# Optimization experiments

Hardware: AMD Instinct MI355X
Metric: run time of the kernel (lower is better)

Reference implementation:

```python
import jax, jax.numpy as jnp
import numpy as np

N_HEADS = 16
D_EMBED = 1024
D_HEADS = D_EMBED // N_HEADS


def setup_inputs() -> dict:
    key = jax.random.key(0)
    k1, k2, k3, k4, k5 = jax.random.split(key, 5)
    B, S = 4, 2048
    x = jax.random.normal(k1, (B, S, D_EMBED), dtype=jnp.float32)
    s_in = 1.0 / np.sqrt(D_EMBED)
    in_proj_w = jax.random.normal(k2, (3 * D_EMBED, D_EMBED), dtype=jnp.float32) * s_in
    in_proj_b = jax.random.normal(k3, (3 * D_EMBED,), dtype=jnp.float32) * 0.01
    out_proj_w = jax.random.normal(k4, (D_EMBED, D_EMBED), dtype=jnp.float32) * s_in
    out_proj_b = jax.random.normal(k5, (D_EMBED,), dtype=jnp.float32) * 0.01
    return {"x": x, "in_proj_w": in_proj_w, "in_proj_b": in_proj_b,
            "out_proj_w": out_proj_w, "out_proj_b": out_proj_b}


def reference(x, in_proj_w, in_proj_b, out_proj_w, out_proj_b):
    B, S, D = x.shape
    # in_proj: Linear(d, 3d); torch chunks output as (k, q, v) in that order
    qkv = jnp.einsum('bsd,ed->bse', x, in_proj_w) + in_proj_b  # [B,S,3D]
    k, q, v = jnp.split(qkv, 3, axis=-1)
    # reshape to heads: [B, H, S, Dh]
    def to_heads(t):
        return t.reshape(B, S, N_HEADS, D_HEADS).transpose(0, 2, 1, 3)
    q, k, v = to_heads(q), to_heads(k), to_heads(v)
    scale = 1.0 / np.sqrt(D_HEADS)
    w = jnp.einsum('bhqd,bhkd->bhqk', q, k) * scale  # [B,H,S,S]
    w = jax.nn.softmax(w, axis=-1)
    score = jnp.einsum('bhqk,bhkd->bhqd', w, v)  # [B,H,S,Dh]
    score = score.transpose(0, 2, 1, 3).reshape(B, S, D)
    out = jnp.einsum('bsd,ed->bse', score, out_proj_w) + out_proj_b
    return out
```

## Files before the change

kernel.cpp:

```cpp
#include <hip/hip_runtime.h>

typedef __attribute__((ext_vector_type(8))) __bf16 bf16x8;
typedef __attribute__((ext_vector_type(4))) float  f32x4;
typedef __attribute__((ext_vector_type(4))) unsigned short us4;

#define QK_SCALE 0.180336880111112f

__device__ __forceinline__ unsigned short f2bf(float f) {
    unsigned u = __float_as_uint(f);
    u += 0x7fffu + ((u >> 16) & 1u);
    return (unsigned short)(u >> 16);
}

__device__ __forceinline__ void gload_lds16(const void* g, void* l) {
    __builtin_amdgcn_global_load_lds((const __attribute__((address_space(1))) void*)g,
                                     (__attribute__((address_space(3))) void*)l, 16, 0, 0);
}

template <int CTRL>
__device__ __forceinline__ float dpp_mov(float x) {
    return __int_as_float(__builtin_amdgcn_update_dpp(0, __float_as_int(x), CTRL, 0xf, 0xf, true));
}
__device__ __forceinline__ float rmax16(float v) {
    v = fmaxf(v, dpp_mov<0x121>(v));
    v = fmaxf(v, dpp_mov<0x122>(v));
    v = fmaxf(v, dpp_mov<0x124>(v));
    v = fmaxf(v, dpp_mov<0x128>(v));
    return v;
}
__device__ __forceinline__ float rsum16(float v) {
    v += dpp_mov<0x121>(v);
    v += dpp_mov<0x122>(v);
    v += dpp_mov<0x124>(v);
    v += dpp_mov<0x128>(v);
    return v;
}

__global__ __launch_bounds__(256) void f32_to_bf16_k(const float* __restrict__ in,
                                                     unsigned short* __restrict__ out, int n) {
    int i = (blockIdx.x * 256 + threadIdx.x) * 4;
    if (i + 3 < n) {
        float4 v = *(const float4*)(in + i);
        us4 o;
        o.x = f2bf(v.x); o.y = f2bf(v.y); o.z = f2bf(v.z); o.w = f2bf(v.w);
        *(us4*)(out + i) = o;
    }
}

__global__ __launch_bounds__(256) void cvt_w1_k(const float* __restrict__ in,
                                                unsigned short* __restrict__ out) {
    int i = (blockIdx.x * 256 + threadIdx.x) * 4;
    float4 v = *(const float4*)(in + i);
    const int row = i >> 10;
    const float s = (row >= 1024 && row < 2048) ? QK_SCALE : 1.0f;
    us4 o;
    o.x = f2bf(v.x * s); o.y = f2bf(v.y * s); o.z = f2bf(v.z * s); o.w = f2bf(v.w * s);
    *(us4*)(out + i) = o;
}

template <int OUTF, int QS>
__global__ __launch_bounds__(256, 2) void gemm_bt(const unsigned short* __restrict__ A,
                                                  const unsigned short* __restrict__ B,
                                                  const float* __restrict__ bias,
                                                  void* __restrict__ Cv,
                                                  int M, int N, int K) {
    __shared__ unsigned short As[4 * 128 * 8];
    __shared__ unsigned short Bs[4 * 128 * 8];
    const int t = threadIdx.x;
    const int lane = t & 63;
    const int w = t >> 6;
    const int wr = w >> 1, wc = w & 1;
    const int lhi = lane >> 4, llo = lane & 15;
    const int bm = blockIdx.y, bn = blockIdx.x;

    f32x4 acc[4][4] = {};

    const unsigned short* Ag = A + (size_t)(bm * 128) * K;
    const unsigned short* Bg = B + (size_t)(bn * 128) * K;

    const int r0 = t & 127, kc0 = t >> 7;
    const int r1 = (256 + t) & 127, kc1 = (256 + t) >> 7;
    const int wbase = (t & ~63) * 8;

    const int KT = K >> 5;
    for (int kt = 0; kt < KT; ++kt) {
        const int k0 = kt * 32;
        gload_lds16(Ag + (size_t)r0 * K + k0 + kc0 * 8, As + wbase);
        gload_lds16(Ag + (size_t)r1 * K + k0 + kc1 * 8, As + 2048 + wbase);
        gload_lds16(Bg + (size_t)r0 * K + k0 + kc0 * 8, Bs + wbase);
        gload_lds16(Bg + (size_t)r1 * K + k0 + kc1 * 8, Bs + 2048 + wbase);
        __syncthreads();

        bf16x8 af[4], bfr[4];
#pragma unroll
        for (int mi = 0; mi < 4; ++mi)
            af[mi] = *(const bf16x8*)(As + lhi * 1024 + (wr * 64 + mi * 16 + llo) * 8);
#pragma unroll
        for (int ni = 0; ni < 4; ++ni)
            bfr[ni] = *(const bf16x8*)(Bs + lhi * 1024 + (wc * 64 + ni * 16 + llo) * 8);
#pragma unroll
        for (int mi = 0; mi < 4; ++mi)
#pragma unroll
            for (int ni = 0; ni < 4; ++ni)
                acc[mi][ni] = __builtin_amdgcn_mfma_f32_16x16x32_bf16(af[mi], bfr[ni], acc[mi][ni], 0, 0, 0);
        __syncthreads();
    }

    const int rowb = bm * 128 + wr * 64;
    const int colb = bn * 128 + wc * 64;
#pragma unroll
    for (int mi = 0; mi < 4; ++mi) {
#pragma unroll
        for (int ni = 0; ni < 4; ++ni) {
            const int col = colb + ni * 16 + llo;
            float bv = bias[col];
            if (QS) bv = (col >= 1024 && col < 2048) ? bv * QK_SCALE : bv;
#pragma unroll
            for (int r = 0; r < 4; ++r) {
                const int row = rowb + mi * 16 + lhi * 4 + r;
                const float v = acc[mi][ni][r] + bv;
                if (OUTF == 0) ((unsigned short*)Cv)[(size_t)row * N + col] = f2bf(v);
                else           ((float*)Cv)[(size_t)row * N + col] = v;
            }
        }
    }
}

__global__ __launch_bounds__(256) void attn_k(const unsigned short* __restrict__ qkv,
                                              unsigned short* __restrict__ score) {
    __shared__ unsigned short Ks[2][4096];
    __shared__ unsigned short Vt[64 * 88];
    __shared__ unsigned short Pl[4][16 * 88];

    const int t = threadIdx.x;
    const int lane = t & 63;
    const int w = t >> 6;
    const int lhi = lane >> 4, llo = lane & 15;
    const int b = blockIdx.y >> 4, h = blockIdx.y & 15;
    const int q0 = blockIdx.x * 128;

    const unsigned short* kvb = qkv + (size_t)b * 2048 * 3072 + h * 64;

    bf16x8 qf[2][2];
#pragma unroll
    for (int mf = 0; mf < 2; ++mf) {
        const unsigned short* qp = qkv + (size_t)(b * 2048 + q0 + w * 32 + mf * 16 + llo) * 3072
                                   + 1024 + h * 64 + lhi * 8;
        qf[mf][0] = *(const bf16x8*)qp;
        qf[mf][1] = *(const bf16x8*)(qp + 32);
    }

    f32x4 oacc[2][4] = {};
    float m_[2][4], l_[2][4];
#pragma unroll
    for (int mf = 0; mf < 2; ++mf)
#pragma unroll
        for (int r = 0; r < 4; ++r) { m_[mf][r] = -1e30f; l_[mf][r] = 0.f; }

    const int vp = t & 31, vdc = t >> 5;
    bf16x8 vr0, vr1;

    auto issueK = [&](int kt, int buf) {
        const unsigned short* g = kvb + (size_t)(kt * 64 + (t & 63)) * 3072 + (t >> 6) * 8;
        gload_lds16(g,      &Ks[buf][(t & ~63) * 8]);
        gload_lds16(g + 32, &Ks[buf][2048 + (t & ~63) * 8]);
    };
    auto issueV = [&](int kt) {
        const unsigned short* g = kvb + 2048 + (size_t)(kt * 64 + 2 * vp) * 3072 + vdc * 8;
        vr0 = *(const bf16x8*)g;
        vr1 = *(const bf16x8*)(g + 3072);
    };
    auto writeVt = [&]() {
        union { bf16x8 v; unsigned short u[8]; } a, c;
        a.v = vr0; c.v = vr1;
        unsigned int* V32 = (unsigned int*)Vt;
#pragma unroll
        for (int j = 0; j < 8; ++j)
            V32[(vdc * 8 + j) * 44 + vp] = (unsigned int)a.u[j] | ((unsigned int)c.u[j] << 16);
    };

    issueK(0, 0);
    __builtin_amdgcn_sched_barrier(0);
    issueV(0);

    for (int kt = 0; kt < 32; ++kt) {
        const int cur = kt & 1;
        if (kt < 31) issueK(kt + 1, cur ^ 1);
        __builtin_amdgcn_sched_barrier(0);
        writeVt();
        if (kt < 31) issueV(kt + 1);
        asm volatile("s_waitcnt lgkmcnt(0)" ::: "memory");
        __builtin_amdgcn_sched_barrier(0);
        __builtin_amdgcn_s_barrier();
        __builtin_amdgcn_sched_barrier(0);

        f32x4 sa[2][4] = {};
#pragma unroll
        for (int ds = 0; ds < 2; ++ds) {
#pragma unroll
            for (int nf = 0; nf < 4; ++nf) {
                bf16x8 kb = *(const bf16x8*)(&Ks[cur][(ds * 4 + lhi) * 512 + (nf * 16 + llo) * 8]);
                sa[0][nf] = __builtin_amdgcn_mfma_f32_16x16x32_bf16(qf[0][ds], kb, sa[0][nf], 0, 0, 0);
                sa[1][nf] = __builtin_amdgcn_mfma_f32_16x16x32_bf16(qf[1][ds], kb, sa[1][nf], 0, 0, 0);
            }
        }

        bf16x8 pa[2][2];
        unsigned short* pw = Pl[w];
#pragma unroll
        for (int mf = 0; mf < 2; ++mf) {
#pragma unroll
            for (int r = 0; r < 4; ++r) {
                float pm = fmaxf(fmaxf(sa[mf][0][r], sa[mf][1][r]), fmaxf(sa[mf][2][r], sa[mf][3][r]));
                pm = rmax16(pm);
                const float mn = fmaxf(m_[mf][r], pm);
                const float c = __builtin_amdgcn_exp2f(m_[mf][r] - mn);
                m_[mf][r] = mn;
                const float p0 = __builtin_amdgcn_exp2f(sa[mf][0][r] - mn);
                const float p1 = __builtin_amdgcn_exp2f(sa[mf][1][r] - mn);
                const float p2 = __builtin_amdgcn_exp2f(sa[mf][2][r] - mn);
                const float p3 = __builtin_amdgcn_exp2f(sa[mf][3][r] - mn);
                sa[mf][0][r] = p0; sa[mf][1][r] = p1; sa[mf][2][r] = p2; sa[mf][3][r] = p3;
                l_[mf][r] = l_[mf][r] * c + (p0 + p1 + p2 + p3);
#pragma unroll
                for (int nf = 0; nf < 4; ++nf) oacc[mf][nf][r] *= c;
            }
#pragma unroll
            for (int nf = 0; nf < 4; ++nf) {
                const int pc = (nf * 16 + llo + (lhi << 4)) & 63;
#pragma unroll
                for (int r = 0; r < 4; ++r)
                    pw[(lhi * 4 + r) * 88 + pc] = f2bf(sa[mf][nf][r]);
            }
            const int xr = (llo & 12) << 2;
            pa[mf][0] = *(const bf16x8*)(pw + llo * 88 + ((lhi * 8 + xr) & 63));
            pa[mf][1] = *(const bf16x8*)(pw + llo * 88 + ((32 + lhi * 8 + xr) & 63));
        }

#pragma unroll
        for (int ks = 0; ks < 2; ++ks) {
#pragma unroll
            for (int nf = 0; nf < 4; ++nf) {
                bf16x8 vb = *(const bf16x8*)(Vt + (nf * 16 + llo) * 88 + ks * 32 + lhi * 8);
                oacc[0][nf] = __builtin_amdgcn_mfma_f32_16x16x32_bf16(pa[0][ks], vb, oacc[0][nf], 0, 0, 0);
                oacc[1][nf] = __builtin_amdgcn_mfma_f32_16x16x32_bf16(pa[1][ks], vb, oacc[1][nf], 0, 0, 0);
            }
        }
        __builtin_amdgcn_sched_barrier(0);
        __builtin_amdgcn_s_barrier();
        __builtin_amdgcn_sched_barrier(0);
    }

#pragma unroll
    for (int mf = 0; mf < 2; ++mf) {
#pragma unroll
        for (int r = 0; r < 4; ++r) {
            const float L = rsum16(l_[mf][r]);
            const float rl = 1.0f / L;
            const int row = b * 2048 + q0 + w * 32 + mf * 16 + lhi * 4 + r;
#pragma unroll
            for (int nf = 0; nf < 4; ++nf)
                score[(size_t)row * 1024 + h * 64 + nf * 16 + llo] = f2bf(oacc[mf][nf][r] * rl);
        }
    }
}

extern "C" void kernel_launch(void* const* d_in, const int* in_sizes, int n_in,
                              void* d_out, int out_size, void* d_ws, size_t ws_size,
                              hipStream_t stream) {
    const float* x  = (const float*)d_in[0];
    const float* w1 = (const float*)d_in[1];
    const float* b1 = (const float*)d_in[2];
    const float* w2 = (const float*)d_in[3];
    const float* b2 = (const float*)d_in[4];
    float* out = (float*)d_out;

    char* ws = (char*)d_ws;
    unsigned short* qkv   = (unsigned short*)ws;
    unsigned short* xbf   = (unsigned short*)(ws + 50331648);
    unsigned short* w1bf  = (unsigned short*)(ws + 50331648 + 16777216);
    unsigned short* w2bf  = (unsigned short*)(ws + 50331648 + 16777216 + 6291456);
    unsigned short* score = xbf;

    f32_to_bf16_k<<<dim3(8388608 / 1024), dim3(256), 0, stream>>>(x,  xbf,  8388608);
    cvt_w1_k<<<dim3(3145728 / 1024), dim3(256), 0, stream>>>(w1, w1bf);
    f32_to_bf16_k<<<dim3(1048576 / 1024), dim3(256), 0, stream>>>(w2, w2bf, 1048576);

    gemm_bt<0, 1><<<dim3(24, 64), dim3(256), 0, stream>>>(xbf, w1bf, b1, (void*)qkv, 8192, 3072, 1024);
    attn_k<<<dim3(16, 64), dim3(256), 0, stream>>>(qkv, score);
    gemm_bt<1, 0><<<dim3(8, 64), dim3(256), 0, stream>>>(score, w2bf, b2, (void*)out, 8192, 1024, 1024);
}
```

Before: 321.5 us.

## Lazy softmax rescale, packed bf16 P stores, and permuted V/P key layout

Skips the online-softmax max update and accumulator rescale unless some row max grows by more than a threshold of 8 (in log2 units), which removes the per-tile rescale multiplies and correction exps in the common case. It also converts P to bf16 with the hardware packed-convert instruction and writes four values at once instead of scalar rounding and per-element stores. To make that possible, the key order inside each tile is permuted consistently for both P columns and V rows (interleaved halves), so the P·V contraction stays correct. The cost is a wave-level vote and branch per tile, and exps can reach up to 2^8 before rescaling, which reduces fp32/bf16 headroom slightly.

```diff
diff --git a/kernel.cpp b/kernel.cpp
--- a/kernel.cpp
+++ b/kernel.cpp
@@ -3,6 +3,7 @@
 typedef __attribute__((ext_vector_type(8))) __bf16 bf16x8;
 typedef __attribute__((ext_vector_type(4))) float  f32x4;
 typedef __attribute__((ext_vector_type(4))) unsigned short us4;
+typedef __attribute__((ext_vector_type(2))) unsigned int u32x2;
 
 #define QK_SCALE 0.180336880111112f
 
@@ -10,6 +11,12 @@
     unsigned u = __float_as_uint(f);
     u += 0x7fffu + ((u >> 16) & 1u);
     return (unsigned short)(u >> 16);
+}
+
+__device__ __forceinline__ unsigned cvt_pk_bf16(float lo, float hi) {
+    unsigned r;
+    asm("v_cvt_pk_bf16_f32 %0, %1, %2" : "=v"(r) : "v"(lo), "v"(hi));
+    return r;
 }
 
 __device__ __forceinline__ void gload_lds16(const void* g, void* l) {
@@ -157,26 +164,28 @@
 #pragma unroll
         for (int r = 0; r < 4; ++r) { m_[mf][r] = -1e30f; l_[mf][r] = 0.f; }
 
-    const int vp = t & 31, vdc = t >> 5;
+    const int c = t & 31, vdc = t >> 5;
+    const int kA = ((c & 1) << 5) + (c >> 1);
+    const unsigned short* vsrc = kvb + 2048 + (size_t)kA * 3072 + vdc * 8;
     bf16x8 vr0, vr1;
 
     auto issueK = [&](int kt, int buf) {
-        const unsigned short* g = kvb + (size_t)(kt * 64 + (t & 63)) * 3072 + (t >> 6) * 8;
+        const unsigned short* g = kvb + (size_t)(kt * 64 + lane) * 3072 + w * 8;
         gload_lds16(g,      &Ks[buf][(t & ~63) * 8]);
         gload_lds16(g + 32, &Ks[buf][2048 + (t & ~63) * 8]);
     };
     auto issueV = [&](int kt) {
-        const unsigned short* g = kvb + 2048 + (size_t)(kt * 64 + 2 * vp) * 3072 + vdc * 8;
+        const unsigned short* g = vsrc + (size_t)kt * 64 * 3072;
         vr0 = *(const bf16x8*)g;
-        vr1 = *(const bf16x8*)(g + 3072);
+        vr1 = *(const bf16x8*)(g + 16 * 3072);
     };
     auto writeVt = [&]() {
-        union { bf16x8 v; unsigned short u[8]; } a, c;
-        a.v = vr0; c.v = vr1;
+        union { bf16x8 v; unsigned short u[8]; } a_, c_;
+        a_.v = vr0; c_.v = vr1;
         unsigned int* V32 = (unsigned int*)Vt;
 #pragma unroll
         for (int j = 0; j < 8; ++j)
-            V32[(vdc * 8 + j) * 44 + vp] = (unsigned int)a.u[j] | ((unsigned int)c.u[j] << 16);
+            V32[(vdc * 8 + j) * 44 + c] = (unsigned int)a_.u[j] | ((unsigned int)c_.u[j] << 16);
     };
 
     issueK(0, 0);
@@ -205,36 +214,61 @@
             }
         }
 
+        float pm[2][4];
+        bool grow = false;
+#pragma unroll
+        for (int mf = 0; mf < 2; ++mf)
+#pragma unroll
+            for (int r = 0; r < 4; ++r) {
+                float q = fmaxf(fmaxf(sa[mf][0][r], sa[mf][1][r]), fmaxf(sa[mf][2][r], sa[mf][3][r]));
+                q = rmax16(q);
+                pm[mf][r] = q;
+                grow = grow || (q > m_[mf][r] + 8.f);
+            }
+        if (__any(grow)) {
+#pragma unroll
+            for (int mf = 0; mf < 2; ++mf)
+#pragma unroll
+                for (int r = 0; r < 4; ++r) {
+                    const float mn = fmaxf(m_[mf][r], pm[mf][r]);
+                    const float cc = __builtin_amdgcn_exp2f(m_[mf][r] - mn);
+                    m_[mf][r] = mn;
+                    const float p0 = __builtin_amdgcn_exp2f(sa[mf][0][r] - mn);
+                    const float p1 = __builtin_amdgcn_exp2f(sa[mf][1][r] - mn);
+                    const float p2 = __builtin_amdgcn_exp2f(sa[mf][2][r] - mn);
+                    const float p3 = __builtin_amdgcn_exp2f(sa[mf][3][r] - mn);
+                    sa[mf][0][r] = p0; sa[mf][1][r] = p1; sa[mf][2][r] = p2; sa[mf][3][r] = p3;
+                    l_[mf][r] = l_[mf][r] * cc + (p0 + p1 + p2 + p3);
+#pragma unroll
+                    for (int nf = 0; nf < 4; ++nf) oacc[mf][nf][r] *= cc;
+                }
+        } else {
+#pragma unroll
+            for (int mf = 0; mf < 2; ++mf)
+#pragma unroll
+                for (int r = 0; r < 4; ++r) {
+                    const float p0 = __builtin_amdgcn_exp2f(sa[mf][0][r] - m_[mf][r]);
+                    const float p1 = __builtin_amdgcn_exp2f(sa[mf][1][r] - m_[mf][r]);
+                    const float p2 = __builtin_amdgcn_exp2f(sa[mf][2][r] - m_[mf][r]);
+                    const float p3 = __builtin_amdgcn_exp2f(sa[mf][3][r] - m_[mf][r]);
+                    sa[mf][0][r] = p0; sa[mf][1][r] = p1; sa[mf][2][r] = p2; sa[mf][3][r] = p3;
+                    l_[mf][r] += (p0 + p1 + p2 + p3);
+                }
+        }
+
         bf16x8 pa[2][2];
         unsigned short* pw = Pl[w];
 #pragma unroll
         for (int mf = 0; mf < 2; ++mf) {
 #pragma unroll
             for (int r = 0; r < 4; ++r) {
-                float pm = fmaxf(fmaxf(sa[mf][0][r], sa[mf][1][r]), fmaxf(sa[mf][2][r], sa[mf][3][r]));
-                pm = rmax16(pm);
-                const float mn = fmaxf(m_[mf][r], pm);
-                const float c = __builtin_amdgcn_exp2f(m_[mf][r] - mn);
-                m_[mf][r] = mn;
-                const float p0 = __builtin_amdgcn_exp2f(sa[mf][0][r] - mn);
-                const float p1 = __builtin_amdgcn_exp2f(sa[mf][1][r] - mn);
-                const float p2 = __builtin_amdgcn_exp2f(sa[mf][2][r] - mn);
-                const float p3 = __builtin_amdgcn_exp2f(sa[mf][3][r] - mn);
-                sa[mf][0][r] = p0; sa[mf][1][r] = p1; sa[mf][2][r] = p2; sa[mf][3][r] = p3;
-                l_[mf][r] = l_[mf][r] * c + (p0 + p1 + p2 + p3);
-#pragma unroll
-                for (int nf = 0; nf < 4; ++nf) oacc[mf][nf][r] *= c;
-            }
-#pragma unroll
-            for (int nf = 0; nf < 4; ++nf) {
-                const int pc = (nf * 16 + llo + (lhi << 4)) & 63;
-#pragma unroll
-                for (int r = 0; r < 4; ++r)
-                    pw[(lhi * 4 + r) * 88 + pc] = f2bf(sa[mf][nf][r]);
-            }
-            const int xr = (llo & 12) << 2;
-            pa[mf][0] = *(const bf16x8*)(pw + llo * 88 + ((lhi * 8 + xr) & 63));
-            pa[mf][1] = *(const bf16x8*)(pw + llo * 88 + ((32 + lhi * 8 + xr) & 63));
+                u32x2 val;
+                val.x = cvt_pk_bf16(sa[mf][0][r], sa[mf][1][r]);
+                val.y = cvt_pk_bf16(sa[mf][2][r], sa[mf][3][r]);
+                *(u32x2*)&pw[(lhi * 4 + r) * 88 + llo * 4] = val;
+            }
+            pa[mf][0] = *(const bf16x8*)(pw + llo * 88 + lhi * 8);
+            pa[mf][1] = *(const bf16x8*)(pw + llo * 88 + 32 + lhi * 8);
         }
 
 #pragma unroll
```

Result: slower. 330.3 us (+2.7%).

## Keep P in registers via transposed QK^T and permuted V rows, lazy rescale

Applied to the files above, without the earlier changes.

The attention kernel now computes S^T (K as the A operand), so each lane holds the probabilities of one query row in a layout that packs directly into the PV MFMA A-operand with v_cvt_pk_bf16. This removes the per-wave LDS round trip for P, and V rows are loaded in a permuted order to match. V^T is double-buffered, which drops one block barrier per iteration, and K prefetch is issued after the barrier with finer vmcnt waits. The online-softmax rescale is skipped unless the running max grows by more than a threshold, which cuts exp and multiply work. The cost is cross-lane shuffles to broadcast scale factors and extra LDS for the second V buffer.

```diff
diff --git a/kernel.cpp b/kernel.cpp
--- a/kernel.cpp
+++ b/kernel.cpp
@@ -12,28 +12,15 @@
     return (unsigned short)(u >> 16);
 }
 
+__device__ __forceinline__ unsigned cvt_pk_bf16(float lo, float hi) {
+    unsigned r;
+    asm("v_cvt_pk_bf16_f32 %0, %1, %2" : "=v"(r) : "v"(lo), "v"(hi));
+    return r;
+}
+
 __device__ __forceinline__ void gload_lds16(const void* g, void* l) {
     __builtin_amdgcn_global_load_lds((const __attribute__((address_space(1))) void*)g,
                                      (__attribute__((address_space(3))) void*)l, 16, 0, 0);
-}
-
-template <int CTRL>
-__device__ __forceinline__ float dpp_mov(float x) {
-    return __int_as_float(__builtin_amdgcn_update_dpp(0, __float_as_int(x), CTRL, 0xf, 0xf, true));
-}
-__device__ __forceinline__ float rmax16(float v) {
-    v = fmaxf(v, dpp_mov<0x121>(v));
-    v = fmaxf(v, dpp_mov<0x122>(v));
-    v = fmaxf(v, dpp_mov<0x124>(v));
-    v = fmaxf(v, dpp_mov<0x128>(v));
-    return v;
-}
-__device__ __forceinline__ float rsum16(float v) {
-    v += dpp_mov<0x121>(v);
-    v += dpp_mov<0x122>(v);
-    v += dpp_mov<0x124>(v);
-    v += dpp_mov<0x128>(v);
-    return v;
 }
 
 __global__ __launch_bounds__(256) void f32_to_bf16_k(const float* __restrict__ in,
@@ -129,8 +116,7 @@
 __global__ __launch_bounds__(256) void attn_k(const unsigned short* __restrict__ qkv,
                                               unsigned short* __restrict__ score) {
     __shared__ unsigned short Ks[2][4096];
-    __shared__ unsigned short Vt[64 * 88];
-    __shared__ unsigned short Pl[4][16 * 88];
+    __shared__ unsigned short Vt[2][5632];
 
     const int t = threadIdx.x;
     const int lane = t & 63;
@@ -151,116 +137,139 @@
     }
 
     f32x4 oacc[2][4] = {};
-    float m_[2][4], l_[2][4];
-#pragma unroll
-    for (int mf = 0; mf < 2; ++mf)
-#pragma unroll
-        for (int r = 0; r < 4; ++r) { m_[mf][r] = -1e30f; l_[mf][r] = 0.f; }
-
-    const int vp = t & 31, vdc = t >> 5;
+    float m_[2] = {-1e30f, -1e30f}, l_[2] = {0.f, 0.f};
+
+    const int c = t & 31, vdc = t >> 5;
+    const int kA = 4 * ((c >> 2) & 3) + 2 * (c & 1) + 16 * (2 * (c >> 4) + ((c >> 1) & 1));
+    const unsigned short* vp = kvb + 2048 + (size_t)kA * 3072 + vdc * 8;
+    const unsigned short* kp = kvb + (size_t)lane * 3072 + w * 8;
     bf16x8 vr0, vr1;
 
-    auto issueK = [&](int kt, int buf) {
-        const unsigned short* g = kvb + (size_t)(kt * 64 + (t & 63)) * 3072 + (t >> 6) * 8;
-        gload_lds16(g,      &Ks[buf][(t & ~63) * 8]);
-        gload_lds16(g + 32, &Ks[buf][2048 + (t & ~63) * 8]);
-    };
-    auto issueV = [&](int kt) {
-        const unsigned short* g = kvb + 2048 + (size_t)(kt * 64 + 2 * vp) * 3072 + vdc * 8;
-        vr0 = *(const bf16x8*)g;
-        vr1 = *(const bf16x8*)(g + 3072);
-    };
-    auto writeVt = [&]() {
-        union { bf16x8 v; unsigned short u[8]; } a, c;
-        a.v = vr0; c.v = vr1;
-        unsigned int* V32 = (unsigned int*)Vt;
-#pragma unroll
-        for (int j = 0; j < 8; ++j)
-            V32[(vdc * 8 + j) * 44 + vp] = (unsigned int)a.u[j] | ((unsigned int)c.u[j] << 16);
-    };
-
-    issueK(0, 0);
-    __builtin_amdgcn_sched_barrier(0);
-    issueV(0);
+    gload_lds16(kp,      &Ks[0][(t & ~63) * 8]);
+    gload_lds16(kp + 32, &Ks[0][2048 + (t & ~63) * 8]);
+    kp += 196608;
+    vr0 = *(const bf16x8*)vp;
+    vr1 = *(const bf16x8*)(vp + 3072);
+    vp += 196608;
 
     for (int kt = 0; kt < 32; ++kt) {
         const int cur = kt & 1;
-        if (kt < 31) issueK(kt + 1, cur ^ 1);
+        {
+            union { bf16x8 v; unsigned short u[8]; } A_, B_;
+            A_.v = vr0; B_.v = vr1;
+            unsigned* V32 = (unsigned*)&Vt[cur][0];
+#pragma unroll
+            for (int j = 0; j < 8; ++j)
+                V32[(vdc * 8 + j) * 44 + c] = (unsigned)A_.u[j] | ((unsigned)B_.u[j] << 16);
+        }
         __builtin_amdgcn_sched_barrier(0);
-        writeVt();
-        if (kt < 31) issueV(kt + 1);
-        asm volatile("s_waitcnt lgkmcnt(0)" ::: "memory");
+        if (kt < 31) {
+            vr0 = *(const bf16x8*)vp;
+            vr1 = *(const bf16x8*)(vp + 3072);
+            vp += 196608;
+        }
         __builtin_amdgcn_sched_barrier(0);
+        if (kt < 31) asm volatile("s_waitcnt vmcnt(2) lgkmcnt(0)" ::: "memory");
+        else         asm volatile("s_waitcnt vmcnt(0) lgkmcnt(0)" ::: "memory");
         __builtin_amdgcn_s_barrier();
         __builtin_amdgcn_sched_barrier(0);
+        if (kt < 31) {
+            gload_lds16(kp,      &Ks[cur ^ 1][(t & ~63) * 8]);
+            gload_lds16(kp + 32, &Ks[cur ^ 1][2048 + (t & ~63) * 8]);
+            kp += 196608;
+        }
 
         f32x4 sa[2][4] = {};
 #pragma unroll
         for (int ds = 0; ds < 2; ++ds) {
 #pragma unroll
+            for (int nfk = 0; nfk < 4; ++nfk) {
+                bf16x8 kb = *(const bf16x8*)(&Ks[cur][(ds * 4 + lhi) * 512 + (nfk * 16 + llo) * 8]);
+                sa[0][nfk] = __builtin_amdgcn_mfma_f32_16x16x32_bf16(kb, qf[0][ds], sa[0][nfk], 0, 0, 0);
+                sa[1][nfk] = __builtin_amdgcn_mfma_f32_16x16x32_bf16(kb, qf[1][ds], sa[1][nfk], 0, 0, 0);
+            }
+        }
+
+        float pmv[2];
+#pragma unroll
+        for (int mf = 0; mf < 2; ++mf) {
+            float p0 = fmaxf(fmaxf(sa[mf][0][0], sa[mf][0][1]), fmaxf(sa[mf][0][2], sa[mf][0][3]));
+            float p1 = fmaxf(fmaxf(sa[mf][1][0], sa[mf][1][1]), fmaxf(sa[mf][1][2], sa[mf][1][3]));
+            float p2 = fmaxf(fmaxf(sa[mf][2][0], sa[mf][2][1]), fmaxf(sa[mf][2][2], sa[mf][2][3]));
+            float p3 = fmaxf(fmaxf(sa[mf][3][0], sa[mf][3][1]), fmaxf(sa[mf][3][2], sa[mf][3][3]));
+            float pm = fmaxf(fmaxf(p0, p1), fmaxf(p2, p3));
+            pm = fmaxf(pm, __shfl_xor(pm, 16, 64));
+            pm = fmaxf(pm, __shfl_xor(pm, 32, 64));
+            pmv[mf] = pm;
+        }
+        const bool grow = (pmv[0] > m_[0] + 8.f) || (pmv[1] > m_[1] + 8.f);
+        if (__any(grow)) {
+#pragma unroll
+            for (int mf = 0; mf < 2; ++mf) {
+                const float mn = fmaxf(m_[mf], pmv[mf]);
+                const float cc = __builtin_amdgcn_exp2f(m_[mf] - mn);
+                m_[mf] = mn;
+                l_[mf] *= cc;
+                const float c0 = __shfl(cc, lhi * 4 + 0, 64);
+                const float c1 = __shfl(cc, lhi * 4 + 1, 64);
+                const float c2 = __shfl(cc, lhi * 4 + 2, 64);
+                const float c3 = __shfl(cc, lhi * 4 + 3, 64);
+#pragma unroll
+                for (int nf = 0; nf < 4; ++nf) {
+                    oacc[mf][nf][0] *= c0; oacc[mf][nf][1] *= c1;
+                    oacc[mf][nf][2] *= c2; oacc[mf][nf][3] *= c3;
+                }
+            }
+        }
+
+        bf16x8 pa[2][2];
+#pragma unroll
+        for (int mf = 0; mf < 2; ++mf) {
+            float p[4][4], s = 0.f;
+#pragma unroll
+            for (int nf = 0; nf < 4; ++nf)
+#pragma unroll
+                for (int r = 0; r < 4; ++r) {
+                    p[nf][r] = __builtin_amdgcn_exp2f(sa[mf][nf][r] - m_[mf]);
+                    s += p[nf][r];
+                }
+            l_[mf] += s;
+            union { unsigned u[4]; bf16x8 v; } k0, k1;
+            k0.u[0] = cvt_pk_bf16(p[0][0], p[0][1]); k0.u[1] = cvt_pk_bf16(p[0][2], p[0][3]);
+            k0.u[2] = cvt_pk_bf16(p[1][0], p[1][1]); k0.u[3] = cvt_pk_bf16(p[1][2], p[1][3]);
+            k1.u[0] = cvt_pk_bf16(p[2][0], p[2][1]); k1.u[1] = cvt_pk_bf16(p[2][2], p[2][3]);
+            k1.u[2] = cvt_pk_bf16(p[3][0], p[3][1]); k1.u[3] = cvt_pk_bf16(p[3][2], p[3][3]);
+            pa[mf][0] = k0.v; pa[mf][1] = k1.v;
+        }
+
+#pragma unroll
+        for (int ks = 0; ks < 2; ++ks)
+#pragma unroll
             for (int nf = 0; nf < 4; ++nf) {
-                bf16x8 kb = *(const bf16x8*)(&Ks[cur][(ds * 4 + lhi) * 512 + (nf * 16 + llo) * 8]);
-                sa[0][nf] = __builtin_amdgcn_mfma_f32_16x16x32_bf16(qf[0][ds], kb, sa[0][nf], 0, 0, 0);
-                sa[1][nf] = __builtin_amdgcn_mfma_f32_16x16x32_bf16(qf[1][ds], kb, sa[1][nf], 0, 0, 0);
-            }
-        }
-
-        bf16x8 pa[2][2];
-        unsigned short* pw = Pl[w];
-#pragma unroll
-        for (int mf = 0; mf < 2; ++mf) {
-#pragma unroll
-            for (int r = 0; r < 4; ++r) {
-                float pm = fmaxf(fmaxf(sa[mf][0][r], sa[mf][1][r]), fmaxf(sa[mf][2][r], sa[mf][3][r]));
-                pm = rmax16(pm);
-                const float mn = fmaxf(m_[mf][r], pm);
-                const float c = __builtin_amdgcn_exp2f(m_[mf][r] - mn);
-                m_[mf][r] = mn;
-                const float p0 = __builtin_amdgcn_exp2f(sa[mf][0][r] - mn);
-                const float p1 = __builtin_amdgcn_exp2f(sa[mf][1][r] - mn);
-                const float p2 = __builtin_amdgcn_exp2f(sa[mf][2][r] - mn);
-                const float p3 = __builtin_amdgcn_exp2f(sa[mf][3][r] - mn);
-                sa[mf][0][r] = p0; sa[mf][1][r] = p1; sa[mf][2][r] = p2; sa[mf][3][r] = p3;
-                l_[mf][r] = l_[mf][r] * c + (p0 + p1 + p2 + p3);
-#pragma unroll
-                for (int nf = 0; nf < 4; ++nf) oacc[mf][nf][r] *= c;
-            }
-#pragma unroll
-            for (int nf = 0; nf < 4; ++nf) {
-                const int pc = (nf * 16 + llo + (lhi << 4)) & 63;
-#pragma unroll
-                for (int r = 0; r < 4; ++r)
-                    pw[(lhi * 4 + r) * 88 + pc] = f2bf(sa[mf][nf][r]);
-            }
-            const int xr = (llo & 12) << 2;
-            pa[mf][0] = *(const bf16x8*)(pw + llo * 88 + ((lhi * 8 + xr) & 63));
-            pa[mf][1] = *(const bf16x8*)(pw + llo * 88 + ((32 + lhi * 8 + xr) & 63));
-        }
-
-#pragma unroll
-        for (int ks = 0; ks < 2; ++ks) {
-#pragma unroll
-            for (int nf = 0; nf < 4; ++nf) {
-                bf16x8 vb = *(const bf16x8*)(Vt + (nf * 16 + llo) * 88 + ks * 32 + lhi * 8);
+                bf16x8 vb = *(const bf16x8*)(&Vt[cur][(nf * 16 + llo) * 88 + ks * 32 + lhi * 8]);
                 oacc[0][nf] = __builtin_amdgcn_mfma_f32_16x16x32_bf16(pa[0][ks], vb, oacc[0][nf], 0, 0, 0);
                 oacc[1][nf] = __builtin_amdgcn_mfma_f32_16x16x32_bf16(pa[1][ks], vb, oacc[1][nf], 0, 0, 0);
             }
-        }
-        __builtin_amdgcn_sched_barrier(0);
-        __builtin_amdgcn_s_barrier();
-        __builtin_amdgcn_sched_barrier(0);
     }
 
 #pragma unroll
     for (int mf = 0; mf < 2; ++mf) {
-#pragma unroll
-        for (int r = 0; r < 4; ++r) {
-            const float L = rsum16(l_[mf][r]);
-            const float rl = 1.0f / L;
-            const int row = b * 2048 + q0 + w * 32 + mf * 16 + lhi * 4 + r;
-#pragma unroll
-            for (int nf = 0; nf < 4; ++nf)
-                score[(size_t)row * 1024 + h * 64 + nf * 16 + llo] = f2bf(oacc[mf][nf][r] * rl);
+        float l = l_[mf];
+        l += __shfl_xor(l, 16, 64);
+        l += __shfl_xor(l, 32, 64);
+        const float rl = 1.0f / l;
+        const float r0 = __shfl(rl, lhi * 4 + 0, 64);
+        const float r1 = __shfl(rl, lhi * 4 + 1, 64);
+        const float r2 = __shfl(rl, lhi * 4 + 2, 64);
+        const float r3 = __shfl(rl, lhi * 4 + 3, 64);
+        const int rowb = b * 2048 + q0 + w * 32 + mf * 16;
+#pragma unroll
+        for (int nf = 0; nf < 4; ++nf) {
+            const int col = h * 64 + nf * 16 + llo;
+            score[(size_t)(rowb + lhi * 4 + 0) * 1024 + col] = f2bf(oacc[mf][nf][0] * r0);
+            score[(size_t)(rowb + lhi * 4 + 1) * 1024 + col] = f2bf(oacc[mf][nf][1] * r1);
+            score[(size_t)(rowb + lhi * 4 + 2) * 1024 + col] = f2bf(oacc[mf][nf][2] * r2);
+            score[(size_t)(rowb + lhi * 4 + 3) * 1024 + col] = f2bf(oacc[mf][nf][3] * r3);
         }
     }
 }
```

After: 283.5 us. -11.8%, faster.
